# Optimization experiments

Measured on AMD Instinct MI355X. Metric: run time of the kernel, lower is better.

The kernel has to match this reference:

```python
import jax, jax.numpy as jnp
import numpy as np

B, S, D, H = 2, 2048, 768, 12
DK = D // H

def setup_inputs() -> dict:
    key = jax.random.key(0)
    ks = jax.random.split(key, 5)
    scale = 1.0 / np.sqrt(D)
    return {
        "X": jax.random.normal(ks[0], (B, S, D), dtype=jnp.float32),
        "Wq": jax.random.normal(ks[1], (D, D), dtype=jnp.float32) * scale,
        "Wk": jax.random.normal(ks[2], (D, D), dtype=jnp.float32) * scale,
        "Wv": jax.random.normal(ks[3], (D, D), dtype=jnp.float32) * scale,
        "Wo": jax.random.normal(ks[4], (D, D), dtype=jnp.float32) * scale,
    }

def reference(X, Wq, Wk, Wv, Wo):
    # torch Linear: y = x @ W.T  (no bias in this repo's Linear)
    Q = X @ Wq.T  # (B,S,D)
    K = X @ Wk.T
    V = X @ Wv.T
    def split_heads(t):
        return t.reshape(B, S, H, DK).transpose(0, 2, 1, 3)  # (B,H,S,DK)
    Qh, Kh, Vh = split_heads(Q), split_heads(K), split_heads(V)
    scores = jnp.einsum('bhqd,bhkd->bhqk', Qh, Kh) / jnp.sqrt(jnp.float32(DK))
    causal = jnp.tril(jnp.ones((S, S), dtype=bool))  # keep lower triangle
    scores = jnp.where(causal, scores, -jnp.inf)
    attn = jax.nn.softmax(scores, axis=-1)
    out_h = jnp.einsum('bhqk,bhkd->bhqd', attn, Vh)  # (B,H,S,DK)
    out = out_h.transpose(0, 2, 1, 3).reshape(B, S, D)
    return out @ Wo.T
```

## Files before the change

kernel.cpp:

```cpp
#include <hip/hip_runtime.h>
#include <stdint.h>

#define BB   2
#define SS   2048
#define DD   768
#define HH   12
#define MM   (BB*SS)
#define XSZ  (MM*DD)
#define WSZ  (DD*DD)

typedef __bf16 v8bf __attribute__((ext_vector_type(8)));
typedef float  v4f  __attribute__((ext_vector_type(4)));

__device__ inline v4f mfma16(v8bf a, v8bf b, v4f c) {
    return __builtin_amdgcn_mfma_f32_16x16x32_bf16(a, b, c, 0, 0, 0);
}

__device__ inline unsigned short f2bf(float f) {
    union { float f; uint32_t u; } v; v.f = f;
    return (unsigned short)((v.u + 0x7FFFu + ((v.u >> 16) & 1u)) >> 16);
}

__device__ inline uint4 cvt8(const float* __restrict__ p) {
    uint4 out;
    unsigned short* s = (unsigned short*)&out;
#pragma unroll
    for (int j = 0; j < 8; ++j) s[j] = f2bf(p[j]);
    return out;
}

__device__ __forceinline__ void gld_lds16(const unsigned short* g, unsigned short* l) {
    __builtin_amdgcn_global_load_lds(
        (const __attribute__((address_space(1))) void*)g,
        (__attribute__((address_space(3))) void*)l, 16, 0, 0);
}

__global__ __launch_bounds__(256) void cvt_x3(
    const float* __restrict__ Wq, const float* __restrict__ Wk,
    const float* __restrict__ Wv, const float* __restrict__ X,
    unsigned short* __restrict__ Wqb,
    unsigned short* __restrict__ Xb)
{
    long i4 = ((long)blockIdx.x * 256 + threadIdx.x) * 4;
    const float* s; unsigned short* d; long off;
    if (i4 < 3L * WSZ) {
        int t = (int)(i4 / WSZ); off = i4 - (long)t * WSZ;
        s = (t == 0) ? Wq : (t == 1) ? Wk : Wv; d = Wqb + (size_t)t * WSZ;
    } else {
        off = i4 - 3L * WSZ; s = X; d = Xb;
    }
    float4 v = *(const float4*)(s + off);
    ushort4 o;
    o.x = f2bf(v.x); o.y = f2bf(v.y); o.z = f2bf(v.z); o.w = f2bf(v.w);
    *(ushort4*)(d + off) = o;
}

__global__ __launch_bounds__(256) void cvt_w3(
    const float* __restrict__ Wq, const float* __restrict__ Wk,
    const float* __restrict__ Wv, unsigned short* __restrict__ dst)
{
    long i4 = ((long)blockIdx.x * 256 + threadIdx.x) * 4;
    int t = (int)(i4 / WSZ);
    long off = i4 - (long)t * WSZ;
    const float* s = (t == 0) ? Wq : (t == 1) ? Wk : Wv;
    float4 v = *(const float4*)(s + off);
    ushort4 o;
    o.x = f2bf(v.x); o.y = f2bf(v.y); o.z = f2bf(v.z); o.w = f2bf(v.w);
    *(ushort4*)(dst + (size_t)t * WSZ + off) = o;
}
__global__ __launch_bounds__(256) void cvt_wo(
    const float* __restrict__ Wo, unsigned short* __restrict__ dst)
{
    long i4 = ((long)blockIdx.x * 256 + threadIdx.x) * 4;
    float4 v = *(const float4*)(Wo + i4);
    ushort4 o;
    o.x = f2bf(v.x); o.y = f2bf(v.y); o.z = f2bf(v.z); o.w = f2bf(v.w);
    *(ushort4*)(dst + i4) = o;
}

__global__ __launch_bounds__(256) void gemm_qkv128(
    const unsigned short* __restrict__ Xb,
    const unsigned short* __restrict__ Wq,
    const unsigned short* __restrict__ Wk,
    const unsigned short* __restrict__ Wv,
    unsigned short* __restrict__ Qo,
    unsigned short* __restrict__ Ko,
    unsigned short* __restrict__ Vo)
{
    __shared__ __align__(16) unsigned short As[128 * 64];
    __shared__ __align__(16) unsigned short Bs[128 * 64];

    const int flat = (int)(blockIdx.y * gridDim.x + blockIdx.x);
    const int sw   = (flat & 7) * 72 + (flat >> 3);
    const int m0   = (sw / 18) * 128;
    const int ncat = (sw % 18) * 128;
    const int z    = ncat / DD;
    const int n0   = ncat - z * DD;

    const unsigned short* W = (z == 0) ? Wq : (z == 1) ? Wk : Wv;

    const int tid  = threadIdx.x;
    const int wave = tid >> 6, lane = tid & 63;
    const int quad = lane >> 4, l16 = lane & 15;
    const int waveM = (wave >> 1) * 64, waveN = (wave & 1) * 64;

    const int rB  = wave * 8 + (lane >> 3);
    const int cB  = ((lane & 7) ^ (lane >> 3)) * 8;
    const int swz = (l16 & 7) << 4;

    v4f acc[4][4] = {};

    const unsigned short* a0 = Xb + (size_t)(m0 + rB) * DD + cB;
    const unsigned short* b0 = W  + (size_t)(n0 + rB) * DD + cB;

    for (int kt = 0; kt < DD; kt += 64) {
        __syncthreads();
#pragma unroll
        for (int c = 0; c < 4; ++c) {
            gld_lds16(a0 + kt + (size_t)(c * 32) * DD, &As[c * 2048 + wave * 512]);
            gld_lds16(b0 + kt + (size_t)(c * 32) * DD, &Bs[c * 2048 + wave * 512]);
        }
        __syncthreads();

#pragma unroll
        for (int kf = 0; kf < 2; ++kf) {
            v8bf af[4], bfr[4];
#pragma unroll
            for (int i = 0; i < 4; ++i) {
                af[i]  = *(const v8bf*)((const char*)As +
                          (size_t)(waveM + i * 16 + l16) * 128 + ((kf * 64 + quad * 16) ^ swz));
                bfr[i] = *(const v8bf*)((const char*)Bs +
                          (size_t)(waveN + i * 16 + l16) * 128 + ((kf * 64 + quad * 16) ^ swz));
            }
#pragma unroll
            for (int mi = 0; mi < 4; ++mi)
#pragma unroll
                for (int ni = 0; ni < 4; ++ni)
                    acc[mi][ni] = mfma16(af[mi], bfr[ni], acc[mi][ni]);
        }
    }

#pragma unroll
    for (int mi = 0; mi < 4; ++mi)
#pragma unroll
        for (int ni = 0; ni < 4; ++ni)
#pragma unroll
            for (int r = 0; r < 4; ++r) {
                const int row = m0 + waveM + mi * 16 + quad * 4 + r;
                const int col = n0 + waveN + ni * 16 + l16;
                const unsigned short val = f2bf(acc[mi][ni][r]);
                if (z == 0)      Qo[(size_t)row * DD + col] = val;
                else if (z == 1) Ko[(size_t)row * DD + col] = val;
                else {
                    const int b = row >> 11, s = row & 2047;
                    const int h = col >> 6,  dk = col & 63;
                    Vo[(((size_t)(b * HH + h)) * 64 + dk) * SS + s] = val;
                }
            }
}

__global__ __launch_bounds__(256) void gemm_qkv64(
    const float* __restrict__ X,
    const unsigned short* __restrict__ Wq,
    const unsigned short* __restrict__ Wk,
    const unsigned short* __restrict__ Wv,
    unsigned short* __restrict__ Qo,
    unsigned short* __restrict__ Ko,
    unsigned short* __restrict__ Vo)
{
    __shared__ __align__(16) unsigned short As[64 * 64];
    __shared__ __align__(16) unsigned short Bs[3][64 * 64];

    const int flat = (int)(blockIdx.y * gridDim.x + blockIdx.x);
    const int sw   = (flat & 7) * 96 + (flat >> 3);
    const int m0   = (sw / 12) * 64;
    const int n0   = (sw % 12) * 64;

    const int tid  = threadIdx.x;
    const int wave = tid >> 6, lane = tid & 63;
    const int quad = lane >> 4, l16 = lane & 15;
    const int waveM = (wave >> 1) * 32, waveN = (wave & 1) * 32;

    const int rA  = tid >> 2;
    const int cA  = (tid & 3) * 16;
    const int rxA = (rA & 7) << 4;

    const int rB  = wave * 8 + (lane >> 3);
    const int cB  = ((lane & 7) ^ (lane >> 3)) * 8;
    const int swz = (l16 & 7) << 4;

    v4f acc[3][2][2] = {};

    const float* ap0 = X + (size_t)(m0 + rA) * DD + cA;
    const unsigned short* w0 = Wq + (size_t)(n0 + rB) * DD + cB;
    const unsigned short* w1 = Wk + (size_t)(n0 + rB) * DD + cB;
    const unsigned short* w2 = Wv + (size_t)(n0 + rB) * DD + cB;

    for (int kt = 0; kt < DD; kt += 64) {
        __syncthreads();
        *(uint4*)((char*)As + rA * 128 + ((cA * 2)      ^ rxA)) = cvt8(ap0 + kt);
        *(uint4*)((char*)As + rA * 128 + ((cA * 2 + 16) ^ rxA)) = cvt8(ap0 + kt + 8);
        gld_lds16(w0 + kt,           &Bs[0][wave * 512]);
        gld_lds16(w0 + kt + 32 * DD, &Bs[0][2048 + wave * 512]);
        gld_lds16(w1 + kt,           &Bs[1][wave * 512]);
        gld_lds16(w1 + kt + 32 * DD, &Bs[1][2048 + wave * 512]);
        gld_lds16(w2 + kt,           &Bs[2][wave * 512]);
        gld_lds16(w2 + kt + 32 * DD, &Bs[2][2048 + wave * 512]);
        __syncthreads();

        v8bf af[2][2];
#pragma unroll
        for (int mi = 0; mi < 2; ++mi) {
            const char* arow = (const char*)As + (size_t)(waveM + mi * 16 + l16) * 128;
#pragma unroll
            for (int kf = 0; kf < 2; ++kf)
                af[mi][kf] = *(const v8bf*)(arow + ((kf * 64 + quad * 16) ^ swz));
        }
#pragma unroll
        for (int z = 0; z < 3; ++z) {
            v8bf bfr[2][2];
#pragma unroll
            for (int ni = 0; ni < 2; ++ni) {
                const char* brow = (const char*)&Bs[z][0] + (size_t)(waveN + ni * 16 + l16) * 128;
#pragma unroll
                for (int kf = 0; kf < 2; ++kf)
                    bfr[ni][kf] = *(const v8bf*)(brow + ((kf * 64 + quad * 16) ^ swz));
            }
#pragma unroll
            for (int mi = 0; mi < 2; ++mi)
#pragma unroll
                for (int ni = 0; ni < 2; ++ni) {
                    acc[z][mi][ni] = mfma16(af[mi][0], bfr[ni][0], acc[z][mi][ni]);
                    acc[z][mi][ni] = mfma16(af[mi][1], bfr[ni][1], acc[z][mi][ni]);
                }
        }
    }

#pragma unroll
    for (int mi = 0; mi < 2; ++mi)
#pragma unroll
        for (int ni = 0; ni < 2; ++ni)
#pragma unroll
            for (int r = 0; r < 4; ++r) {
                const int row = m0 + waveM + mi * 16 + quad * 4 + r;
                const int col = n0 + waveN + ni * 16 + l16;
                Qo[(size_t)row * DD + col] = f2bf(acc[0][mi][ni][r]);
                Ko[(size_t)row * DD + col] = f2bf(acc[1][mi][ni][r]);
                const int b = row >> 11, s = row & 2047;
                const int h = col >> 6,  dk = col & 63;
                Vo[(((size_t)(b * HH + h)) * 64 + dk) * SS + s] = f2bf(acc[2][mi][ni][r]);
            }
}

template<int A_ASYNC, int W_ASYNC, int C_F32>
__global__ __launch_bounds__(256) void gemm_64(
    const void* __restrict__ Ain, const void* __restrict__ W0,
    void* __restrict__ C0)
{
    const int K = DD, N = DD;
    const void* W = W0;
    void* C = C0;

    __shared__ __align__(16) unsigned short As[64 * 32];
    __shared__ __align__(16) unsigned short Bs[64 * 32];

    const int tid  = threadIdx.x;
    const int wave = tid >> 6, lane = tid & 63;
    const int quad = lane >> 4, l16 = lane & 15;
    const int waveM = (wave >> 1) * 32, waveN = (wave & 1) * 32;
    const int m0 = blockIdx.y * 64, n0 = blockIdx.x * 64;

    const int rS = (tid >> 2), cS = (tid & 3) * 8;

    v4f acc[2][2] = {};

    for (int kt = 0; kt < K; kt += 32) {
        __syncthreads();
        if (A_ASYNC)
            gld_lds16((const unsigned short*)Ain + (size_t)(m0 + rS) * K + kt + cS,
                      &As[wave * 512]);
        else
            *(uint4*)(&As[tid * 8]) = cvt8((const float*)Ain + (size_t)(m0 + rS) * K + kt + cS);
        if (W_ASYNC)
            gld_lds16((const unsigned short*)W + (size_t)(n0 + rS) * K + kt + cS,
                      &Bs[wave * 512]);
        else
            *(uint4*)(&Bs[tid * 8]) = cvt8((const float*)W + (size_t)(n0 + rS) * K + kt + cS);
        __syncthreads();

        v8bf af[2], bf[2];
#pragma unroll
        for (int i = 0; i < 2; ++i) {
            af[i] = *(const v8bf*)(&As[(waveM + i * 16 + l16) * 32 + quad * 8]);
            bf[i] = *(const v8bf*)(&Bs[(waveN + i * 16 + l16) * 32 + quad * 8]);
        }
#pragma unroll
        for (int mi = 0; mi < 2; ++mi)
#pragma unroll
            for (int ni = 0; ni < 2; ++ni)
                acc[mi][ni] = mfma16(af[mi], bf[ni], acc[mi][ni]);
    }

#pragma unroll
    for (int mi = 0; mi < 2; ++mi)
#pragma unroll
        for (int ni = 0; ni < 2; ++ni)
#pragma unroll
            for (int r = 0; r < 4; ++r) {
                int row = m0 + waveM + mi * 16 + quad * 4 + r;
                int col = n0 + waveN + ni * 16 + l16;
                if (C_F32) {
                    ((float*)C)[(size_t)row * N + col] = acc[mi][ni][r];
                } else {
                    ((unsigned short*)C)[(size_t)row * N + col] = f2bf(acc[mi][ni][r]);
                }
            }
}

__global__ __launch_bounds__(256, 3) void attn_ls(
    const unsigned short* Q,
    const unsigned short* __restrict__ Kg,
    const unsigned short* __restrict__ Vt,
    unsigned short* O)
{
    const int h = blockIdx.x, b = blockIdx.y;
    const int qs = (SS / 64 - 1 - (int)blockIdx.z) * 64;
    const int tid  = threadIdx.x;
    const int wave = tid >> 6, lane = tid & 63;
    const int quad = lane >> 4, l16 = lane & 15;
    const int qw = qs + wave * 16;
    const float scale = 0.125f;

    __shared__ __align__(16) unsigned short Ks[2][4096];
    __shared__ __align__(16) unsigned short Vs[2][4096];
    __shared__ __align__(16) unsigned short Ps[4][16 * 72];

    v8bf qf0, qf1;
    {
        const unsigned short* qp = &Q[((size_t)(b * SS + qw + l16)) * DD + h * 64];
        qf0 = *(const v8bf*)(qp + quad * 8);
        qf1 = *(const v8bf*)(qp + 32 + quad * 8);
    }

    const int NT = qs / 64 + 1;
    const char* kgb = (const char*)&Kg[(size_t)(b * SS) * DD + h * 64];
    const char* vgb = (const char*)&Vt[((size_t)(b * HH + h) * 64) * SS];

    const int rA = wave * 8 + (lane >> 3);
    const int oA = ((lane & 7) * 16) ^ ((rA & 7) << 4);
    const int swz = (l16 & 7) << 4;

    v4f oacc[4] = {};
    float l_run[4] = {0.f, 0.f, 0.f, 0.f};
    unsigned short* pw = &Ps[wave][0];

    gld_lds16((const unsigned short*)(kgb + (size_t)rA        * (DD * 2) + oA), &Ks[0][wave * 512]);
    gld_lds16((const unsigned short*)(kgb + (size_t)(rA + 32) * (DD * 2) + oA), &Ks[0][2048 + wave * 512]);
    gld_lds16((const unsigned short*)(vgb + (size_t)rA        * (SS * 2) + oA), &Vs[0][wave * 512]);
    gld_lds16((const unsigned short*)(vgb + (size_t)(rA + 32) * (SS * 2) + oA), &Vs[0][2048 + wave * 512]);
    __syncthreads();

    for (int kt = 0; kt < NT; ++kt) {
        const int cur = kt & 1;
        const int kb  = kt * 64;

        if (kt + 1 < NT) {
            const size_t kb2 = (size_t)(kb + 64);
            gld_lds16((const unsigned short*)(kgb + (kb2 + rA)      * (DD * 2) + oA), &Ks[cur ^ 1][wave * 512]);
            gld_lds16((const unsigned short*)(kgb + (kb2 + rA + 32) * (DD * 2) + oA), &Ks[cur ^ 1][2048 + wave * 512]);
            gld_lds16((const unsigned short*)(vgb + (size_t)rA        * (SS * 2) + kb2 * 2 + oA), &Vs[cur ^ 1][wave * 512]);
            gld_lds16((const unsigned short*)(vgb + (size_t)(rA + 32) * (SS * 2) + kb2 * 2 + oA), &Vs[cur ^ 1][2048 + wave * 512]);
        }

        const char* ksb = (const char*)&Ks[cur][0];
        const char* vsb = (const char*)&Vs[cur][0];

        v8bf kf0[4], kf1[4];
#pragma unroll
        for (int nk = 0; nk < 4; ++nk) {
            const char* krow = ksb + (size_t)(nk * 16 + l16) * 128;
            kf0[nk] = *(const v8bf*)(krow + ((quad * 16) ^ swz));
            kf1[nk] = *(const v8bf*)(krow + ((64 + quad * 16) ^ swz));
        }

        v4f sacc[4] = {};
#pragma unroll
        for (int nk = 0; nk < 4; ++nk) {
            sacc[nk] = mfma16(qf0, kf0[nk], sacc[nk]);
            sacc[nk] = mfma16(qf1, kf1[nk], sacc[nk]);
        }

        const bool diag = (kt == NT - 1);
        float pv[4][4];
#pragma unroll
        for (int nk = 0; nk < 4; ++nk)
#pragma unroll
            for (int r = 0; r < 4; ++r) {
                float p = __expf(sacc[nk][r] * scale);
                if (diag) {
                    int key  = kb + nk * 16 + l16;
                    int qrow = qw + quad * 4 + r;
                    if (key > qrow) p = 0.0f;
                }
                pv[nk][r] = p;
                l_run[r] += p;
            }

        v8bf vf[2][4];
#pragma unroll
        for (int kc = 0; kc < 2; ++kc)
#pragma unroll
            for (int dt = 0; dt < 4; ++dt) {
                const char* vr = vsb + (size_t)(dt * 16 + l16) * 128;
                vf[kc][dt] = *(const v8bf*)(vr + ((kc * 64 + quad * 16) ^ swz));
            }

#pragma unroll
        for (int nk = 0; nk < 4; ++nk)
#pragma unroll
            for (int r = 0; r < 4; ++r)
                pw[(quad * 4 + r) * 72 + nk * 16 + l16] = f2bf(pv[nk][r]);
        __asm__ volatile("" ::: "memory");

        v8bf pa0 = *(const v8bf*)(&pw[l16 * 72 + quad * 8]);
        v8bf pa1 = *(const v8bf*)(&pw[l16 * 72 + 32 + quad * 8]);
#pragma unroll
        for (int dt = 0; dt < 4; ++dt) oacc[dt] = mfma16(pa0, vf[0][dt], oacc[dt]);
#pragma unroll
        for (int dt = 0; dt < 4; ++dt) oacc[dt] = mfma16(pa1, vf[1][dt], oacc[dt]);

        __syncthreads();
    }

    for (int off = 1; off < 16; off <<= 1)
#pragma unroll
        for (int r = 0; r < 4; ++r)
            l_run[r] += __shfl_xor(l_run[r], off, 64);

    float inv[4];
#pragma unroll
    for (int r = 0; r < 4; ++r) inv[r] = 1.0f / l_run[r];

    unsigned short* ob = &O[((size_t)(b * SS + qw + quad * 4)) * DD + h * 64 + l16];
#pragma unroll
    for (int r = 0; r < 4; ++r)
#pragma unroll
        for (int dt = 0; dt < 4; ++dt)
            ob[(size_t)r * DD + dt * 16] = f2bf(oacc[dt][r] * inv[r]);
}

extern "C" void kernel_launch(void* const* d_in, const int* in_sizes, int n_in,
                              void* d_out, int out_size, void* d_ws, size_t ws_size,
                              hipStream_t stream)
{
    const float* X  = (const float*)d_in[0];
    const float* Wq = (const float*)d_in[1];
    const float* Wk = (const float*)d_in[2];
    const float* Wv = (const float*)d_in[3];
    const float* Wo = (const float*)d_in[4];
    float* Out = (float*)d_out;

    unsigned short* Qb  = (unsigned short*)d_ws;
    unsigned short* Kb  = Qb + XSZ;
    unsigned short* Xb  = Kb + XSZ;
    unsigned short* Vtb = (unsigned short*)d_out;
    unsigned short* Wqb = Vtb + XSZ;
    unsigned short* Wkb = Wqb + WSZ;
    unsigned short* Wvb = Wkb + WSZ;

    dim3 blk(256);
    dim3 g2(HH, BB, SS / 64);
    dim3 g3(DD / 64, MM / 64);

    if (ws_size >= (size_t)8 * XSZ) {
        cvt_x3<<<4800, blk, 0, stream>>>(Wq, Wk, Wv, X, Wqb, Xb);

        dim3 g1(2304 / 128, MM / 128);
        gemm_qkv128<<<g1, blk, 0, stream>>>(Xb, Wqb, Wkb, Wvb, Qb, Kb, Vtb);

        attn_ls<<<g2, blk, 0, stream>>>(Qb, Kb, Vtb, Qb);

        cvt_wo<<<576, blk, 0, stream>>>(Wo, Kb);

        gemm_64<1, 1, 1><<<g3, blk, 0, stream>>>(Qb, Kb, Out);
    } else {
        cvt_w3<<<1728, blk, 0, stream>>>(Wq, Wk, Wv, Wqb);

        dim3 g1(DD / 64, MM / 64);
        gemm_qkv64<<<g1, blk, 0, stream>>>(X, Wqb, Wkb, Wvb, Qb, Kb, Vtb);

        attn_ls<<<g2, blk, 0, stream>>>(Qb, Kb, Vtb, Qb);

        cvt_wo<<<576, blk, 0, stream>>>(Wo, Kb);

        gemm_64<1, 1, 1><<<g3, blk, 0, stream>>>(Qb, Kb, Out);
    }
}
```

Measured before the change: 173.8 us.

## Double-buffer LDS in QKV and output GEMMs with swizzled 64-wide K tiles

Both the QKV projection GEMM and the output projection GEMM now double-buffer their LDS tiles, issuing async global-to-LDS loads for the next K tile while MFMAs run on the current one. This cuts the per-iteration barrier count to one. The output GEMM is rewritten with 64-wide K tiles, an XOR-swizzled LDS layout and a grouped block-index remap meant to improve L2 reuse. The cost is doubled LDS use per block, which may lower occupancy for the 128x128 QKV kernel.

```diff
diff --git a/kernel.cpp b/kernel.cpp
--- a/kernel.cpp
+++ b/kernel.cpp
@@ -87,8 +87,8 @@
     unsigned short* __restrict__ Ko,
     unsigned short* __restrict__ Vo)
 {
-    __shared__ __align__(16) unsigned short As[128 * 64];
-    __shared__ __align__(16) unsigned short Bs[128 * 64];
+    __shared__ __align__(16) unsigned short As[2][128 * 64];
+    __shared__ __align__(16) unsigned short Bs[2][128 * 64];
 
     const int flat = (int)(blockIdx.y * gridDim.x + blockIdx.x);
     const int sw   = (flat & 7) * 72 + (flat >> 3);
@@ -113,23 +113,32 @@
     const unsigned short* a0 = Xb + (size_t)(m0 + rB) * DD + cB;
     const unsigned short* b0 = W  + (size_t)(n0 + rB) * DD + cB;
 
+#pragma unroll
+    for (int c = 0; c < 4; ++c) {
+        gld_lds16(a0 + (size_t)(c * 32) * DD, &As[0][c * 2048 + wave * 512]);
+        gld_lds16(b0 + (size_t)(c * 32) * DD, &Bs[0][c * 2048 + wave * 512]);
+    }
+    __syncthreads();
+
+    int cur = 0;
     for (int kt = 0; kt < DD; kt += 64) {
-        __syncthreads();
-#pragma unroll
-        for (int c = 0; c < 4; ++c) {
-            gld_lds16(a0 + kt + (size_t)(c * 32) * DD, &As[c * 2048 + wave * 512]);
-            gld_lds16(b0 + kt + (size_t)(c * 32) * DD, &Bs[c * 2048 + wave * 512]);
-        }
-        __syncthreads();
-
+        if (kt + 64 < DD) {
+#pragma unroll
+            for (int c = 0; c < 4; ++c) {
+                gld_lds16(a0 + kt + 64 + (size_t)(c * 32) * DD,
+                          &As[cur ^ 1][c * 2048 + wave * 512]);
+                gld_lds16(b0 + kt + 64 + (size_t)(c * 32) * DD,
+                          &Bs[cur ^ 1][c * 2048 + wave * 512]);
+            }
+        }
 #pragma unroll
         for (int kf = 0; kf < 2; ++kf) {
             v8bf af[4], bfr[4];
 #pragma unroll
             for (int i = 0; i < 4; ++i) {
-                af[i]  = *(const v8bf*)((const char*)As +
+                af[i]  = *(const v8bf*)((const char*)&As[cur][0] +
                           (size_t)(waveM + i * 16 + l16) * 128 + ((kf * 64 + quad * 16) ^ swz));
-                bfr[i] = *(const v8bf*)((const char*)Bs +
+                bfr[i] = *(const v8bf*)((const char*)&Bs[cur][0] +
                           (size_t)(waveN + i * 16 + l16) * 128 + ((kf * 64 + quad * 16) ^ swz));
             }
 #pragma unroll
@@ -138,6 +147,8 @@
                 for (int ni = 0; ni < 4; ++ni)
                     acc[mi][ni] = mfma16(af[mi], bfr[ni], acc[mi][ni]);
         }
+        __syncthreads();
+        cur ^= 1;
     }
 
 #pragma unroll
@@ -252,53 +263,65 @@
             }
 }
 
-template<int A_ASYNC, int W_ASYNC, int C_F32>
-__global__ __launch_bounds__(256) void gemm_64(
-    const void* __restrict__ Ain, const void* __restrict__ W0,
-    void* __restrict__ C0)
-{
-    const int K = DD, N = DD;
-    const void* W = W0;
-    void* C = C0;
-
-    __shared__ __align__(16) unsigned short As[64 * 32];
-    __shared__ __align__(16) unsigned short Bs[64 * 32];
+__global__ __launch_bounds__(256) void gemm_o(
+    const unsigned short* __restrict__ A,
+    const unsigned short* __restrict__ W,
+    float* __restrict__ C)
+{
+    __shared__ __align__(16) unsigned short As[2][64 * 64];
+    __shared__ __align__(16) unsigned short Bs[2][64 * 64];
+
+    const int flat = (int)(blockIdx.y * gridDim.x + blockIdx.x);
+    const int sw   = (flat & 7) * 96 + (flat >> 3);
+    const int m0   = (sw / 12) * 64;
+    const int n0   = (sw % 12) * 64;
 
     const int tid  = threadIdx.x;
     const int wave = tid >> 6, lane = tid & 63;
     const int quad = lane >> 4, l16 = lane & 15;
     const int waveM = (wave >> 1) * 32, waveN = (wave & 1) * 32;
-    const int m0 = blockIdx.y * 64, n0 = blockIdx.x * 64;
-
-    const int rS = (tid >> 2), cS = (tid & 3) * 8;
+
+    const int rB  = wave * 8 + (lane >> 3);
+    const int cB  = ((lane & 7) ^ (lane >> 3)) * 8;
+    const int swz = (l16 & 7) << 4;
+
+    const unsigned short* a0 = A + (size_t)(m0 + rB) * DD + cB;
+    const unsigned short* b0 = W + (size_t)(n0 + rB) * DD + cB;
 
     v4f acc[2][2] = {};
 
-    for (int kt = 0; kt < K; kt += 32) {
+    gld_lds16(a0,           &As[0][wave * 512]);
+    gld_lds16(a0 + 32 * DD, &As[0][2048 + wave * 512]);
+    gld_lds16(b0,           &Bs[0][wave * 512]);
+    gld_lds16(b0 + 32 * DD, &Bs[0][2048 + wave * 512]);
+    __syncthreads();
+
+    int cur = 0;
+    for (int kt = 0; kt < DD; kt += 64) {
+        if (kt + 64 < DD) {
+            gld_lds16(a0 + kt + 64,           &As[cur ^ 1][wave * 512]);
+            gld_lds16(a0 + kt + 64 + 32 * DD, &As[cur ^ 1][2048 + wave * 512]);
+            gld_lds16(b0 + kt + 64,           &Bs[cur ^ 1][wave * 512]);
+            gld_lds16(b0 + kt + 64 + 32 * DD, &Bs[cur ^ 1][2048 + wave * 512]);
+        }
+#pragma unroll
+        for (int kf = 0; kf < 2; ++kf) {
+            v8bf af[2], bfr[2];
+#pragma unroll
+            for (int i = 0; i < 2; ++i) {
+                af[i]  = *(const v8bf*)((const char*)&As[cur][0] +
+                          (size_t)(waveM + i * 16 + l16) * 128 + ((kf * 64 + quad * 16) ^ swz));
+                bfr[i] = *(const v8bf*)((const char*)&Bs[cur][0] +
+                          (size_t)(waveN + i * 16 + l16) * 128 + ((kf * 64 + quad * 16) ^ swz));
+            }
+#pragma unroll
+            for (int mi = 0; mi < 2; ++mi)
+#pragma unroll
+                for (int ni = 0; ni < 2; ++ni)
+                    acc[mi][ni] = mfma16(af[mi], bfr[ni], acc[mi][ni]);
+        }
         __syncthreads();
-        if (A_ASYNC)
-            gld_lds16((const unsigned short*)Ain + (size_t)(m0 + rS) * K + kt + cS,
-                      &As[wave * 512]);
-        else
-            *(uint4*)(&As[tid * 8]) = cvt8((const float*)Ain + (size_t)(m0 + rS) * K + kt + cS);
-        if (W_ASYNC)
-            gld_lds16((const unsigned short*)W + (size_t)(n0 + rS) * K + kt + cS,
-                      &Bs[wave * 512]);
-        else
-            *(uint4*)(&Bs[tid * 8]) = cvt8((const float*)W + (size_t)(n0 + rS) * K + kt + cS);
-        __syncthreads();
-
-        v8bf af[2], bf[2];
-#pragma unroll
-        for (int i = 0; i < 2; ++i) {
-            af[i] = *(const v8bf*)(&As[(waveM + i * 16 + l16) * 32 + quad * 8]);
-            bf[i] = *(const v8bf*)(&Bs[(waveN + i * 16 + l16) * 32 + quad * 8]);
-        }
-#pragma unroll
-        for (int mi = 0; mi < 2; ++mi)
-#pragma unroll
-            for (int ni = 0; ni < 2; ++ni)
-                acc[mi][ni] = mfma16(af[mi], bf[ni], acc[mi][ni]);
+        cur ^= 1;
     }
 
 #pragma unroll
@@ -307,13 +330,9 @@
         for (int ni = 0; ni < 2; ++ni)
 #pragma unroll
             for (int r = 0; r < 4; ++r) {
-                int row = m0 + waveM + mi * 16 + quad * 4 + r;
-                int col = n0 + waveN + ni * 16 + l16;
-                if (C_F32) {
-                    ((float*)C)[(size_t)row * N + col] = acc[mi][ni][r];
-                } else {
-                    ((unsigned short*)C)[(size_t)row * N + col] = f2bf(acc[mi][ni][r]);
-                }
+                const int row = m0 + waveM + mi * 16 + quad * 4 + r;
+                const int col = n0 + waveN + ni * 16 + l16;
+                C[(size_t)row * DD + col] = acc[mi][ni][r];
             }
 }
 
@@ -482,7 +501,7 @@
 
         cvt_wo<<<576, blk, 0, stream>>>(Wo, Kb);
 
-        gemm_64<1, 1, 1><<<g3, blk, 0, stream>>>(Qb, Kb, Out);
+        gemm_o<<<g3, blk, 0, stream>>>(Qb, Kb, Out);
     } else {
         cvt_w3<<<1728, blk, 0, stream>>>(Wq, Wk, Wv, Wqb);
 
@@ -493,6 +512,6 @@
 
         cvt_wo<<<576, blk, 0, stream>>>(Wo, Kb);
 
-        gemm_64<1, 1, 1><<<g3, blk, 0, stream>>>(Qb, Kb, Out);
-    }
-}
+        gemm_o<<<g3, blk, 0, stream>>>(Qb, Kb, Out);
+    }
+}
```

Result: faster. 168.4 us (-3.1%).
